# Kernel tuning notes

Measured on AMD Instinct MI355X. Metric: run time of the kernel, lower is better.

Reference implementation:

```python
import jax, jax.numpy as jnp
import numpy as np

N = 6144          # atoms (~300 residues)
K = 6             # sequence-separation bins (k_vals clamped to 0..5)
T = 85            # RASP 'all' atom types
D = 21            # distance bins -> max_d = 20 A
NBRE_NT_EXCLU = 2 # exclude pairs with residue separation <= 2
N_RES = 307


def setup_inputs() -> dict:
    key = jax.random.key(0)
    k1, k2, k3, k4, k5 = jax.random.split(key, 5)
    # coords scaled so pair distances populate the 0..20 A bin range
    coords = jax.random.normal(k1, (N, 3), jnp.float32) * 5.0
    # atoms grouped by residue -> sorted residue ids
    res_ids = jnp.sort(jax.random.randint(k2, (N,), 0, N_RES)).astype(jnp.int32)
    types = jax.random.randint(k3, (N,), 0, T).astype(jnp.int32)
    types = jnp.where(jax.random.uniform(k4, (N,)) < 0.02, jnp.int32(-1), types)
    pot_tensor = jax.random.normal(k5, (K, T, T, D), jnp.float32) * 0.5
    return {"coords": coords, "res_ids": res_ids, "types": types, "pot_tensor": pot_tensor}


def reference(coords, res_ids, types, pot_tensor):
    n = coords.shape[0]
    # static upper-triangular pair indices (i < j), as in torch.triu_indices(offset=1)
    ii_np, jj_np = np.triu_indices(n, k=1)
    ii = jnp.asarray(ii_np, jnp.int32)
    jj = jnp.asarray(jj_np, jnp.int32)

    sep = jnp.abs(res_ids[ii] - res_ids[jj])                       # [P]
    mask = (sep > NBRE_NT_EXCLU) & (types[ii] != -1) & (types[jj] != -1)

    diff = coords[ii] - coords[jj]                                 # [P,3]
    dists = jnp.sqrt(jnp.sum(diff * diff, axis=1)) + 1e-8          # [P]

    k_vals = jnp.clip(sep - 1, 0, 5)
    max_d = pot_tensor.shape[3] - 1
    d0 = jnp.floor(jnp.clip(dists, 0, max_d)).astype(jnp.int32)
    d1 = jnp.minimum(d0 + 1, max_d)
    alpha = dists - d0.astype(dists.dtype)

    # masked pairs may carry type -1; redirect their gather to index 0
    # (their contribution is zeroed by `mask` below, matching torch semantics)
    ti = jnp.where(mask, types[ii], 0)
    tj = jnp.where(mask, types[jj], 0)

    e0 = pot_tensor[k_vals, ti, tj, d0]                            # [P] 4D gather
    e1 = pot_tensor[k_vals, ti, tj, d1]

    contrib = ((1.0 - alpha) * e0 + alpha * e1 - 2.7)
    contrib = contrib * (dists < max_d).astype(contrib.dtype) * mask.astype(contrib.dtype)
    return jnp.sum(contrib)
```

## Files before the change

kernel.cpp:

```cpp
#include <hip/hip_runtime.h>


#define T_TYPES 85
#define D_BINS 21
#define KSTRIDE (T_TYPES * T_TYPES * D_BINS)
#define NKEYS 86
#define TILE 128
#define PAIR_THREADS 256
#define JCHUNK 64

__global__ __launch_bounds__(1024) void sort_kernel(const float* __restrict__ coords,
                                                    const int* __restrict__ res_ids,
                                                    const int* __restrict__ types,
                                                    int n, int npad,
                                                    float4* __restrict__ sorted,
                                                    float* __restrict__ out) {
    __shared__ int hist[NKEYS];
    __shared__ int offs[NKEYS];
    int tid = threadIdx.x;
    if (tid < NKEYS) hist[tid] = 0;
    if (tid == 0) *out = 0.0f;
    __syncthreads();
    for (int i = tid; i < n; i += 1024) {
        int t = types[i];
        int key = (t < 0) ? (NKEYS - 1) : t;
        atomicAdd(&hist[key], 1);
    }
    __syncthreads();
    if (tid < NKEYS) {
        int s = 0;
#pragma unroll 1
        for (int k = 0; k < NKEYS; ++k) {
            int h = hist[k];
            s += (k < tid) ? h : 0;
        }
        offs[tid] = s;
    }
    __syncthreads();
    for (int i = tid; i < n; i += 1024) {
        int t = types[i];
        int inv = (t < 0);
        int key = inv ? (NKEYS - 1) : t;
        int pos = atomicAdd(&offs[key], 1);
        float4 v;
        if (inv) {
            v.x = 1e8f * (float)(i + 1);
            v.y = 0.0f;
            v.z = 0.0f;
            v.w = __int_as_float(0);
        } else {
            v.x = coords[3 * i + 0];
            v.y = coords[3 * i + 1];
            v.z = coords[3 * i + 2];
            v.w = __int_as_float((res_ids[i] << 11) | (t * D_BINS));
        }
        sorted[pos] = v;
    }
    for (int i = n + tid; i < npad; i += 1024) {
        float4 v;
        v.x = 1e8f * (float)(i + 1);
        v.y = 0.0f;
        v.z = 0.0f;
        v.w = __int_as_float(0);
        sorted[i] = v;
    }
}

template <bool DIAG>
__device__ __forceinline__ float tile_accum(const float4* __restrict__ jt,
                                            float4 mine, int resi, int tbase,
                                            int j0, int p, int q0,
                                            const float* __restrict__ pot) {
    float acc = 0.0f;
#pragma unroll 8
    for (int u = 0; u < JCHUNK; ++u) {
        int jj = j0 + u;
        float4 o = jt[jj];
        float dx = mine.x - o.x;
        float dy = mine.y - o.y;
        float dz = mine.z - o.z;
        float d2 = __builtin_fmaf(dx, dx, __builtin_fmaf(dy, dy, dz * dz));
        float dist = __builtin_amdgcn_sqrtf(d2) + 1e-8f;

        int packj = __float_as_int(o.w);
        int resj = packj >> 11;
        int kj21 = packj & 0x7FF;
        int sep = resi - resj;
        sep = (sep < 0) ? -sep : sep;

        int valid = (sep > 2) & (dist < 20.0f);
        if (DIAG) valid &= ((q0 + jj) > p);

        int k = sep - 1;
        k = (k > 5) ? 5 : k;
        int d0i = (int)dist;
        d0i = (d0i > 19) ? 19 : d0i;
        float alpha = dist - (float)d0i;

        int idx = k * KSTRIDE + (tbase + kj21 + d0i);
        idx = valid ? idx : 0;
        float e0 = pot[idx];
        float e1 = pot[idx + 1];
        float val = __builtin_fmaf(alpha, e1 - e0, e0) - 2.7f;
        acc += valid ? val : 0.0f;
    }
    return acc;
}

__global__ __launch_bounds__(PAIR_THREADS, 6) void pair_kernel(const float4* __restrict__ sorted,
                                                               const float* __restrict__ pot,
                                                               int nt,
                                                               float* __restrict__ out) {
    __shared__ float4 jtile[TILE];
    __shared__ float wsum[PAIR_THREADS / 64];

    int b = blockIdx.x;
    int bi = (int)((2.0 * nt + 1.0 -
                    sqrt((2.0 * nt + 1.0) * (2.0 * nt + 1.0) - 8.0 * (double)b)) * 0.5);
    if (bi < 0) bi = 0;
    if (bi > nt - 1) bi = nt - 1;
    while ((bi + 1) * nt - ((bi + 1) * bi) / 2 <= b) ++bi;
    while (bi * nt - (bi * (bi - 1)) / 2 > b) --bi;
    int bj = bi + (b - (bi * nt - (bi * (bi - 1)) / 2));

    int tid = threadIdx.x;
    int ilane = tid & (TILE - 1);
    int chunk = tid >> 7;
    int q0 = bj * TILE;
    int p = bi * TILE + ilane;

    float4 mine = sorted[p];
    if (tid < TILE) jtile[tid] = sorted[q0 + tid];
    __syncthreads();

    int packi = __float_as_int(mine.w);
    int resi = packi >> 11;
    int tbase = (packi & 0x7FF) * T_TYPES;
    int j0 = chunk * JCHUNK;

    float acc;
    if (bi == bj)
        acc = tile_accum<true>(jtile, mine, resi, tbase, j0, p, q0, pot);
    else
        acc = tile_accum<false>(jtile, mine, resi, tbase, j0, p, q0, pot);

#pragma unroll
    for (int off = 32; off > 0; off >>= 1)
        acc += __shfl_down(acc, off, 64);
    int wave = tid >> 6;
    if ((tid & 63) == 0) wsum[wave] = acc;
    __syncthreads();
    if (tid == 0) {
        float s = wsum[0] + wsum[1] + wsum[2] + wsum[3];
        atomicAdd(out, s);
    }
}

extern "C" void kernel_launch(void* const* d_in, const int* in_sizes, int n_in,
                              void* d_out, int out_size, void* d_ws, size_t ws_size,
                              hipStream_t stream) {
    const float* coords = (const float*)d_in[0];
    const int* res_ids = (const int*)d_in[1];
    const int* types   = (const int*)d_in[2];
    const float* pot   = (const float*)d_in[3];
    int n = in_sizes[1];
    float* out = (float*)d_out;

    float4* sorted = (float4*)d_ws;

    int nt = (n + TILE - 1) / TILE;
    int npad = nt * TILE;
    sort_kernel<<<1, 1024, 0, stream>>>(coords, res_ids, types, n, npad, sorted, out);

    int nblocks = nt * (nt + 1) / 2;
    pair_kernel<<<nblocks, PAIR_THREADS, 0, stream>>>(sorted, pot, nt, out);
}
```

Before: 94.49 us.

## Read j-tile directly from global sorted buffer instead of LDS staging

```diff
diff --git a/kernel.cpp b/kernel.cpp
--- a/kernel.cpp
+++ b/kernel.cpp
@@ -8,12 +8,14 @@
 #define TILE 128
 #define PAIR_THREADS 256
 #define JCHUNK 64
+#define MAXN 8192
+
+__device__ float4 g_sorted[MAXN];
 
 __global__ __launch_bounds__(1024) void sort_kernel(const float* __restrict__ coords,
                                                     const int* __restrict__ res_ids,
                                                     const int* __restrict__ types,
                                                     int n, int npad,
-                                                    float4* __restrict__ sorted,
                                                     float* __restrict__ out) {
     __shared__ int hist[NKEYS];
     __shared__ int offs[NKEYS];
@@ -21,10 +23,17 @@
     if (tid < NKEYS) hist[tid] = 0;
     if (tid == 0) *out = 0.0f;
     __syncthreads();
-    for (int i = tid; i < n; i += 1024) {
+    int n4 = n >> 2;
+    for (int i = tid; i < n4; i += 1024) {
+        int4 tv = ((const int4*)types)[i];
+        atomicAdd(&hist[(tv.x < 0) ? (NKEYS - 1) : tv.x], 1);
+        atomicAdd(&hist[(tv.y < 0) ? (NKEYS - 1) : tv.y], 1);
+        atomicAdd(&hist[(tv.z < 0) ? (NKEYS - 1) : tv.z], 1);
+        atomicAdd(&hist[(tv.w < 0) ? (NKEYS - 1) : tv.w], 1);
+    }
+    for (int i = (n4 << 2) + tid; i < n; i += 1024) {
         int t = types[i];
-        int key = (t < 0) ? (NKEYS - 1) : t;
-        atomicAdd(&hist[key], 1);
+        atomicAdd(&hist[(t < 0) ? (NKEYS - 1) : t], 1);
     }
     __syncthreads();
     if (tid < NKEYS) {
@@ -54,7 +63,7 @@
             v.z = coords[3 * i + 2];
             v.w = __int_as_float((res_ids[i] << 11) | (t * D_BINS));
         }
-        sorted[pos] = v;
+        g_sorted[pos] = v;
     }
     for (int i = n + tid; i < npad; i += 1024) {
         float4 v;
@@ -62,20 +71,19 @@
         v.y = 0.0f;
         v.z = 0.0f;
         v.w = __int_as_float(0);
-        sorted[i] = v;
+        g_sorted[i] = v;
     }
 }
 
 template <bool DIAG>
-__device__ __forceinline__ float tile_accum(const float4* __restrict__ jt,
-                                            float4 mine, int resi, int tbase,
+__device__ __forceinline__ float tile_accum(float4 mine, int resi, int tbase,
                                             int j0, int p, int q0,
                                             const float* __restrict__ pot) {
     float acc = 0.0f;
 #pragma unroll 8
     for (int u = 0; u < JCHUNK; ++u) {
         int jj = j0 + u;
-        float4 o = jt[jj];
+        float4 o = g_sorted[q0 + jj];
         float dx = mine.x - o.x;
         float dy = mine.y - o.y;
         float dz = mine.z - o.z;
@@ -107,11 +115,9 @@
     return acc;
 }
 
-__global__ __launch_bounds__(PAIR_THREADS, 6) void pair_kernel(const float4* __restrict__ sorted,
-                                                               const float* __restrict__ pot,
+__global__ __launch_bounds__(PAIR_THREADS, 6) void pair_kernel(const float* __restrict__ pot,
                                                                int nt,
                                                                float* __restrict__ out) {
-    __shared__ float4 jtile[TILE];
     __shared__ float wsum[PAIR_THREADS / 64];
 
     int b = blockIdx.x;
@@ -129,9 +135,7 @@
     int q0 = bj * TILE;
     int p = bi * TILE + ilane;
 
-    float4 mine = sorted[p];
-    if (tid < TILE) jtile[tid] = sorted[q0 + tid];
-    __syncthreads();
+    float4 mine = g_sorted[p];
 
     int packi = __float_as_int(mine.w);
     int resi = packi >> 11;
@@ -140,9 +144,9 @@
 
     float acc;
     if (bi == bj)
-        acc = tile_accum<true>(jtile, mine, resi, tbase, j0, p, q0, pot);
+        acc = tile_accum<true>(mine, resi, tbase, j0, p, q0, pot);
     else
-        acc = tile_accum<false>(jtile, mine, resi, tbase, j0, p, q0, pot);
+        acc = tile_accum<false>(mine, resi, tbase, j0, p, q0, pot);
 
 #pragma unroll
     for (int off = 32; off > 0; off >>= 1)
@@ -166,12 +170,11 @@
     int n = in_sizes[1];
     float* out = (float*)d_out;
 
-    float4* sorted = (float4*)d_ws;
-
     int nt = (n + TILE - 1) / TILE;
     int npad = nt * TILE;
-    sort_kernel<<<1, 1024, 0, stream>>>(coords, res_ids, types, n, npad, sorted, out);
+
+    sort_kernel<<<1, 1024, 0, stream>>>(coords, res_ids, types, n, npad, out);
 
     int nblocks = nt * (nt + 1) / 2;
-    pair_kernel<<<nblocks, PAIR_THREADS, 0, stream>>>(sorted, pot, nt, out);
+    pair_kernel<<<nblocks, PAIR_THREADS, 0, stream>>>(pot, nt, out);
 }
```

Result: slower. 98.89 us (+4.7%).
